# Optimization experiments

Hardware: AMD Instinct MI355X
Metric: run time of the kernel (lower is better)

Reference implementation:

```python
import jax, jax.numpy as jnp
import numpy as np

N_NODES = 8192

def setup_inputs() -> dict:
    key = jax.random.key(0)
    k1, k2, k3 = jax.random.split(key, 3)
    x = jax.random.normal(k1, (N_NODES, 256), dtype=jnp.float32)
    edge_index = jax.random.randint(k2, (2, 262144), 0, N_NODES, dtype=jnp.int64)
    W = jax.random.normal(k3, (256, 128), dtype=jnp.float32) / np.sqrt(256.0)
    b = jnp.zeros((128,), dtype=jnp.float32)
    return {"x": x, "edge_index": edge_index, "W": W, "b": b}

def reference(x, edge_index, W, b):
    # PyG GCNConv: h = X W; add self-loops; sym-normalize D^-1/2 (A+I) D^-1/2; aggregate; + bias
    N = x.shape[0]
    h = x @ W  # [N, H]
    loops = jnp.arange(N, dtype=edge_index.dtype)
    src = jnp.concatenate([edge_index[0], loops])  # [E+N]
    dst = jnp.concatenate([edge_index[1], loops])
    deg = jax.ops.segment_sum(jnp.ones_like(dst, dtype=h.dtype), dst, num_segments=N)  # in-degree incl. self-loop
    dinv = jax.lax.rsqrt(deg)  # deg >= 1 due to self-loops
    norm = dinv[src] * dinv[dst]  # [E+N]
    msgs = h[src] * norm[:, None]  # gather + scale
    agg = jax.ops.segment_sum(msgs, dst, num_segments=N)  # scatter-add to targets
    z = jax.nn.relu(agg + b)  # [N, H]
    adj_recon = jax.nn.sigmoid(z @ z.T)  # [N, N]
    return adj_recon, z
```

## Files before the change

### kernel.cpp

```cpp
#include <hip/hip_runtime.h>
#include <hip/hip_bf16.h>

#define N_NODES 8192
#define E_EDGES 262144
#define HID 128
#define FIN 256
#define CAP 128

typedef __attribute__((ext_vector_type(8))) short bf16x8;
typedef __attribute__((ext_vector_type(4))) float f32x4;

__global__ __launch_bounds__(256) void xw_kernel(const float* __restrict__ x,
                                                 const float* __restrict__ W,
                                                 float* __restrict__ h,
                                                 unsigned* __restrict__ cursor) {
    if (blockIdx.x < 32) cursor[blockIdx.x * 256 + threadIdx.x] = 0u;

    int col = threadIdx.x & 127;
    int row0 = blockIdx.x * 16 + (threadIdx.x >> 7) * 8;
    const float* xr = x + (size_t)row0 * FIN;
    float acc[8];
#pragma unroll
    for (int r = 0; r < 8; ++r) acc[r] = 0.f;

    for (int k = 0; k < FIN; k += 4) {
        float4 xv[8];
#pragma unroll
        for (int r = 0; r < 8; ++r) xv[r] = *(const float4*)(xr + r * FIN + k);
#pragma unroll
        for (int kk = 0; kk < 4; ++kk) {
            float w = W[(size_t)(k + kk) * HID + col];
#pragma unroll
            for (int r = 0; r < 8; ++r)
                acc[r] = fmaf(((const float*)&xv[r])[kk], w, acc[r]);
        }
    }
#pragma unroll
    for (int r = 0; r < 8; ++r)
        h[(size_t)(row0 + r) * HID + col] = acc[r];
}

__global__ void scatter_csr(const int* __restrict__ src, const int* __restrict__ dst,
                            unsigned* __restrict__ cursor, int* __restrict__ csr_src) {
    int e = blockIdx.x * 256 + threadIdx.x;
    if (e < E_EDGES) {
        int d = dst[e];
        unsigned pos = atomicAdd(&cursor[d], 1u);
        csr_src[(size_t)d * CAP + pos] = src[e];
    }
}

__global__ __launch_bounds__(256) void agg_kernel(const float* __restrict__ h,
                                                  const unsigned* __restrict__ cnt,
                                                  const int* __restrict__ csr_src,
                                                  const float* __restrict__ b,
                                                  float* __restrict__ z_out,
                                                  __hip_bfloat16* __restrict__ zb) {
    int row = blockIdx.x;
    int slot = threadIdx.x >> 6;
    int fp = threadIdx.x & 63;
    const float2* h2 = (const float2*)h;
    const int* bin = csr_src + (size_t)row * CAP;

    unsigned ne = cnt[row];
    float ax = 0.f, ay = 0.f;
    for (unsigned base = (unsigned)slot * 8; base < ne; base += 32) {
        int4 i0 = *(const int4*)(bin + base);
        int4 i1 = *(const int4*)(bin + base + 4);
        int ss[8] = {i0.x, i0.y, i0.z, i0.w, i1.x, i1.y, i1.z, i1.w};
        unsigned rem = ne - base;
#pragma unroll
        for (int j = 0; j < 8; ++j) {
            int s = ((unsigned)j < rem) ? ss[j] : ss[0];
            float ds = rsqrtf((float)(cnt[s] + 1u));
            ds = ((unsigned)j < rem) ? ds : 0.f;
            float2 hv = h2[(size_t)s * 64 + fp];
            ax = fmaf(hv.x, ds, ax);
            ay = fmaf(hv.y, ds, ay);
        }
    }
    __shared__ float part[4][64][2];
    part[slot][fp][0] = ax;
    part[slot][fp][1] = ay;
    __syncthreads();
    if (slot == 0) {
        float di = rsqrtf((float)(ne + 1u));
        float2 hv = h2[(size_t)row * 64 + fp];
        float sx = (part[0][fp][0] + part[1][fp][0]) + (part[2][fp][0] + part[3][fp][0]) + hv.x * di;
        float sy = (part[0][fp][1] + part[1][fp][1]) + (part[2][fp][1] + part[3][fp][1]) + hv.y * di;
        float2 bb = ((const float2*)b)[fp];
        float zx = fmaxf(fmaf(sx, di, bb.x), 0.f);
        float zy = fmaxf(fmaf(sy, di, bb.y), 0.f);
        ((float2*)z_out)[(size_t)row * 64 + fp] = make_float2(zx, zy);
        unsigned short bx = __builtin_bit_cast(unsigned short, __float2bfloat16(zx));
        unsigned short by = __builtin_bit_cast(unsigned short, __float2bfloat16(zy));
        ((unsigned*)zb)[(size_t)row * 64 + fp] = ((unsigned)by << 16) | (unsigned)bx;
    }
}

__global__ __launch_bounds__(256) void gemm_sig(const __hip_bfloat16* __restrict__ zb,
                                                float* __restrict__ adj) {
    int strip = blockIdx.x & 7;
    int p = blockIdx.x >> 3;
    int TI = 0, rem = p;
    while (rem >= 16 - TI) { rem -= 16 - TI; ++TI; }
    int TJ = TI + rem;

    int wid = threadIdx.x >> 6;
    int lane = threadIdx.x & 63;
    int lr = lane & 15;
    int hi = lane >> 4;
    int lk = hi * 8;

    int row0 = TI * 512 + strip * 64;
    int col0 = TJ * 512 + wid * 128;

    f32x4 acc[4][8];
#pragma unroll
    for (int m = 0; m < 4; ++m)
#pragma unroll
        for (int n = 0; n < 8; ++n) acc[m][n] = (f32x4){0.f, 0.f, 0.f, 0.f};

#pragma unroll
    for (int ks = 0; ks < 4; ++ks) {
        int k = ks * 32 + lk;
        bf16x8 a[4], bfr[8];
#pragma unroll
        for (int m = 0; m < 4; ++m)
            a[m] = *(const bf16x8*)(zb + (size_t)(row0 + m * 16 + lr) * HID + k);
#pragma unroll
        for (int n = 0; n < 8; ++n)
            bfr[n] = *(const bf16x8*)(zb + (size_t)(col0 + n * 16 + lr) * HID + k);
#pragma unroll
        for (int m = 0; m < 4; ++m)
#pragma unroll
            for (int n = 0; n < 8; ++n)
                acc[m][n] = __builtin_amdgcn_mfma_f32_16x16x32_bf16(a[m], bfr[n], acc[m][n], 0, 0, 0);
    }

    int orow = hi * 4;
    bool mirror = (TI != TJ);
#pragma unroll
    for (int m = 0; m < 4; ++m) {
        int rowb = row0 + m * 16 + orow;
#pragma unroll
        for (int n = 0; n < 8; ++n) {
            int col = col0 + n * 16 + lr;
            f32x4 s4;
#pragma unroll
            for (int r = 0; r < 4; ++r) {
                float v = acc[m][n][r];
                s4[r] = __builtin_amdgcn_rcpf(1.0f + __expf(-v));
            }
#pragma unroll
            for (int r = 0; r < 4; ++r)
                adj[(size_t)(rowb + r) * N_NODES + col] = s4[r];
            if (mirror)
                __builtin_nontemporal_store(s4, (f32x4*)(adj + (size_t)col * N_NODES + rowb));
        }
    }
}

extern "C" void kernel_launch(void* const* d_in, const int* in_sizes, int n_in,
                              void* d_out, int out_size, void* d_ws, size_t ws_size,
                              hipStream_t stream) {
    const float* x = (const float*)d_in[0];
    const int* ei = (const int*)d_in[1];
    const float* W = (const float*)d_in[2];
    const float* b = (const float*)d_in[3];
    const int* src = ei;
    const int* dst = ei + E_EDGES;

    float* adj = (float*)d_out;
    float* z_out = (float*)d_out + (size_t)N_NODES * N_NODES;

    char* ws = (char*)d_ws;
    float* h = (float*)ws;
    __hip_bfloat16* zb = (__hip_bfloat16*)(ws + (4u << 20));
    unsigned* cursor = (unsigned*)(ws + (6u << 20));
    int* csr = (int*)(ws + (6u << 20) + (32u << 10));

    hipLaunchKernelGGL(xw_kernel, dim3(N_NODES / 16), dim3(256), 0, stream, x, W, h, cursor);
    hipLaunchKernelGGL(scatter_csr, dim3(E_EDGES / 256), dim3(256), 0, stream, src, dst, cursor, csr);
    hipLaunchKernelGGL(agg_kernel, dim3(N_NODES), dim3(256), 0, stream, h, cursor, csr, b, z_out, zb);
    hipLaunchKernelGGL(gemm_sig, dim3(136 * 8), dim3(256), 0, stream, zb, adj);
}
```

Before: 134.5 us.

## Replace global-atomic CSR scatter with per-block histogram, scan and placement

```diff
diff --git a/kernel.cpp b/kernel.cpp
--- a/kernel.cpp
+++ b/kernel.cpp
@@ -12,10 +12,7 @@
 
 __global__ __launch_bounds__(256) void xw_kernel(const float* __restrict__ x,
                                                  const float* __restrict__ W,
-                                                 float* __restrict__ h,
-                                                 unsigned* __restrict__ cursor) {
-    if (blockIdx.x < 32) cursor[blockIdx.x * 256 + threadIdx.x] = 0u;
-
+                                                 float* __restrict__ h) {
     int col = threadIdx.x & 127;
     int row0 = blockIdx.x * 16 + (threadIdx.x >> 7) * 8;
     const float* xr = x + (size_t)row0 * FIN;
@@ -40,13 +37,60 @@
         h[(size_t)(row0 + r) * HID + col] = acc[r];
 }
 
-__global__ void scatter_csr(const int* __restrict__ src, const int* __restrict__ dst,
-                            unsigned* __restrict__ cursor, int* __restrict__ csr_src) {
-    int e = blockIdx.x * 256 + threadIdx.x;
-    if (e < E_EDGES) {
-        int d = dst[e];
-        unsigned pos = atomicAdd(&cursor[d], 1u);
-        csr_src[(size_t)d * CAP + pos] = src[e];
+__global__ __launch_bounds__(256) void count_hist(const int* __restrict__ dst,
+                                                  unsigned short* __restrict__ histG) {
+    __shared__ unsigned hist[N_NODES];
+#pragma unroll
+    for (int i = 0; i < N_NODES / 256; ++i) hist[i * 256 + threadIdx.x] = 0u;
+    __syncthreads();
+    int gid = blockIdx.x * 256 + threadIdx.x;
+    int4 d4 = ((const int4*)dst)[gid];
+    atomicAdd(&hist[d4.x], 1u);
+    atomicAdd(&hist[d4.y], 1u);
+    atomicAdd(&hist[d4.z], 1u);
+    atomicAdd(&hist[d4.w], 1u);
+    __syncthreads();
+    size_t base = (size_t)blockIdx.x * N_NODES;
+#pragma unroll
+    for (int i = 0; i < N_NODES / 256; ++i) {
+        int d = i * 256 + threadIdx.x;
+        histG[base + d] = (unsigned short)hist[d];
+    }
+}
+
+__global__ __launch_bounds__(256) void scan_hist(unsigned short* __restrict__ histG,
+                                                 unsigned* __restrict__ deg) {
+    int d = blockIdx.x * 256 + threadIdx.x;
+    unsigned run = 0;
+    for (int b = 0; b < 256; ++b) {
+        size_t idx = (size_t)b * N_NODES + d;
+        unsigned v = histG[idx];
+        histG[idx] = (unsigned short)run;
+        run += v;
+    }
+    deg[d] = run;
+}
+
+__global__ __launch_bounds__(256) void place_csr(const int* __restrict__ src,
+                                                 const int* __restrict__ dst,
+                                                 const unsigned short* __restrict__ histG,
+                                                 int* __restrict__ csr) {
+    __shared__ unsigned lcur[N_NODES];
+#pragma unroll
+    for (int i = 0; i < N_NODES / 256; ++i) lcur[i * 256 + threadIdx.x] = 0u;
+    __syncthreads();
+    int gid = blockIdx.x * 256 + threadIdx.x;
+    int4 s4 = ((const int4*)src)[gid];
+    int4 d4 = ((const int4*)dst)[gid];
+    size_t base = (size_t)blockIdx.x * N_NODES;
+    int ds[4] = {d4.x, d4.y, d4.z, d4.w};
+    int ss[4] = {s4.x, s4.y, s4.z, s4.w};
+#pragma unroll
+    for (int j = 0; j < 4; ++j) {
+        int d = ds[j];
+        unsigned lpos = atomicAdd(&lcur[d], 1u);
+        unsigned gbase = histG[base + d];
+        csr[(size_t)d * CAP + gbase + lpos] = ss[j];
     }
 }
 
@@ -177,11 +221,14 @@
     char* ws = (char*)d_ws;
     float* h = (float*)ws;
     __hip_bfloat16* zb = (__hip_bfloat16*)(ws + (4u << 20));
-    unsigned* cursor = (unsigned*)(ws + (6u << 20));
-    int* csr = (int*)(ws + (6u << 20) + (32u << 10));
-
-    hipLaunchKernelGGL(xw_kernel, dim3(N_NODES / 16), dim3(256), 0, stream, x, W, h, cursor);
-    hipLaunchKernelGGL(scatter_csr, dim3(E_EDGES / 256), dim3(256), 0, stream, src, dst, cursor, csr);
-    hipLaunchKernelGGL(agg_kernel, dim3(N_NODES), dim3(256), 0, stream, h, cursor, csr, b, z_out, zb);
+    unsigned short* histG = (unsigned short*)(ws + (6u << 20));
+    unsigned* deg = (unsigned*)(ws + (10u << 20));
+    int* csr = (int*)(ws + (10u << 20) + (32u << 10));
+
+    hipLaunchKernelGGL(xw_kernel, dim3(N_NODES / 16), dim3(256), 0, stream, x, W, h);
+    hipLaunchKernelGGL(count_hist, dim3(256), dim3(256), 0, stream, dst, histG);
+    hipLaunchKernelGGL(scan_hist, dim3(32), dim3(256), 0, stream, histG, deg);
+    hipLaunchKernelGGL(place_csr, dim3(256), dim3(256), 0, stream, src, dst, histG, csr);
+    hipLaunchKernelGGL(agg_kernel, dim3(N_NODES), dim3(256), 0, stream, h, deg, csr, b, z_out, zb);
     hipLaunchKernelGGL(gemm_sig, dim3(136 * 8), dim3(256), 0, stream, zb, adj);
 }
```

Result: slower. 137.4 us (+2.2%).
